# Kernel tuning notes

Hardware: AMD Instinct MI355X
Metric: run time of the kernel (lower is better)

The kernel has to match this reference:

```python
import jax, jax.numpy as jnp
import numpy as np

D_MODEL = 1024
N_HEADS = 16
HEAD_DIM = D_MODEL // N_HEADS
D_FF = 4096
EPS = 1e-5
THETA = 10000.0
B, S = 2, 2048


def _rope_cache(seq_len, head_dim, theta=THETA):
    inv_freq = 1.0 / theta ** (jnp.arange(0, head_dim, 2, dtype=jnp.float32) / head_dim)
    t = jnp.arange(seq_len, dtype=jnp.float32)
    freqs = jnp.einsum('i,j->ij', t, inv_freq)          # [S, head_dim//2]
    emb = jnp.concatenate([freqs, freqs], axis=-1)       # [S, head_dim]
    return jnp.cos(emb), jnp.sin(emb)


def _rotate_half(x):
    x1, x2 = jnp.split(x, 2, axis=-1)
    return jnp.concatenate([-x2, x1], axis=-1)


def _ada_rmsnorm(x, time_emb, weight, w1, b1, w2, b2):
    # time_mlp: Linear -> SiLU -> Linear producing [B, 2*D]
    h = jax.nn.silu(time_emb @ w1 + b1)
    scale, shift = jnp.split(h @ w2 + b2, 2, axis=-1)    # each [B, D]
    norm = x * jax.lax.rsqrt(jnp.mean(x * x, axis=-1, keepdims=True) + EPS)
    return norm * weight * (1.0 + scale[:, None, :]) + shift[:, None, :]


def setup_inputs() -> dict:
    key = jax.random.key(0)
    ks = jax.random.split(key, 24)
    rn = lambda k, shp: (jax.random.normal(k, shp, dtype=jnp.float32) * 0.02)
    return {
        'x': jax.random.normal(ks[0], (B, S, D_MODEL), dtype=jnp.float32),
        'time_emb': jax.random.normal(ks[1], (B, D_MODEL), dtype=jnp.float32),
        # norm1
        'w_norm1': jnp.ones((D_MODEL,), jnp.float32),
        't1_w1': rn(ks[2], (D_MODEL, D_MODEL)), 't1_b1': jnp.zeros((D_MODEL,), jnp.float32),
        't1_w2': rn(ks[3], (D_MODEL, 2 * D_MODEL)), 't1_b2': jnp.zeros((2 * D_MODEL,), jnp.float32),
        # norm2
        'w_norm2': jnp.ones((D_MODEL,), jnp.float32),
        't2_w1': rn(ks[4], (D_MODEL, D_MODEL)), 't2_b1': jnp.zeros((D_MODEL,), jnp.float32),
        't2_w2': rn(ks[5], (D_MODEL, 2 * D_MODEL)), 't2_b2': jnp.zeros((2 * D_MODEL,), jnp.float32),
        # attention projections (stored [in, out])
        'wq': rn(ks[6], (D_MODEL, D_MODEL)), 'bq': jnp.zeros((D_MODEL,), jnp.float32),
        'wk': rn(ks[7], (D_MODEL, D_MODEL)), 'bk': jnp.zeros((D_MODEL,), jnp.float32),
        'wv': rn(ks[8], (D_MODEL, D_MODEL)), 'bv': jnp.zeros((D_MODEL,), jnp.float32),
        'wo': rn(ks[9], (D_MODEL, D_MODEL)), 'bo': jnp.zeros((D_MODEL,), jnp.float32),
        # GLU FFN (no bias)
        'w_gate': rn(ks[10], (D_MODEL, D_FF)),
        'w_up': rn(ks[11], (D_MODEL, D_FF)),
        'w_down': rn(ks[12], (D_FF, D_MODEL)),
    }


def reference(x, time_emb,
              w_norm1, t1_w1, t1_b1, t1_w2, t1_b2,
              w_norm2, t2_w1, t2_b1, t2_w2, t2_b2,
              wq, bq, wk, bk, wv, bv, wo, bo,
              w_gate, w_up, w_down):
    b, s, _ = x.shape
    cos, sin = _rope_cache(s, HEAD_DIM)                  # [S, head_dim]

    # --- attention sub-block ---
    nx = _ada_rmsnorm(x, time_emb, w_norm1, t1_w1, t1_b1, t1_w2, t1_b2)
    q = (nx @ wq + bq).reshape(b, s, N_HEADS, HEAD_DIM)
    k = (nx @ wk + bk).reshape(b, s, N_HEADS, HEAD_DIM)
    v = (nx @ wv + bv).reshape(b, s, N_HEADS, HEAD_DIM)
    c = cos[:, None, :]  # [S,1,head_dim] broadcasts over heads
    si = sin[:, None, :]
    q = q * c + _rotate_half(q) * si
    k = k * c + _rotate_half(k) * si
    scores = jnp.einsum('bshd,bthd->bhst', q, k) / jnp.sqrt(jnp.float32(HEAD_DIM))
    probs = jax.nn.softmax(scores, axis=-1)
    attn = jnp.einsum('bhst,bthd->bshd', probs, v).reshape(b, s, D_MODEL)
    x = x + attn @ wo + bo

    # --- GLU FFN sub-block ---
    nx = _ada_rmsnorm(x, time_emb, w_norm2, t2_w1, t2_b1, t2_w2, t2_b2)
    gate = jax.nn.gelu(nx @ w_gate, approximate=False)
    ff = (gate * (nx @ w_up)) @ w_down
    return x + ff
```

## Files before the change

### kernel.cpp

```cpp
#include <hip/hip_runtime.h>
#include <hip/hip_bf16.h>

typedef __bf16 bf16_t;
typedef __bf16 bf16x8 __attribute__((ext_vector_type(8)));
typedef float f32x4 __attribute__((ext_vector_type(4)));

typedef __attribute__((address_space(3))) void lds_void_t;
typedef const __attribute__((address_space(1))) void gbl_void_t;

static constexpr int S_LEN = 2048;
static constexpr int NBATCH = 2;
static constexpr int DM = 1024;
static constexpr int NH = 16;
static constexpr int HD = 64;
static constexpr int DFF = 4096;
static constexpr int MROWS = NBATCH * S_LEN;
static constexpr int QKVN = 3072;

__global__ __launch_bounds__(256) void rope_table_k(float* __restrict__ cs) {
  int idx = blockIdx.x * 256 + threadIdx.x;
  int i = idx & 31, s = idx >> 5;
  float inv = powf(10000.0f, -(float)i / 32.0f);
  float ang = (float)s * inv;
  float c = cosf(ang), sn = sinf(ang);
  cs[s * 64 + i] = c;  cs[s * 64 + i + 32] = c;
  cs[S_LEN * 64 + s * 64 + i] = sn;  cs[S_LEN * 64 + s * 64 + i + 32] = sn;
}

__global__ __launch_bounds__(256) void gemv_k(const float* __restrict__ vin,
    const float* __restrict__ W, const float* __restrict__ bias,
    float* __restrict__ out, int N, int dosilu) {
  int b = blockIdx.y;
  int tj = threadIdx.x & 31, ti = threadIdx.x >> 5;
  int j = blockIdx.x * 32 + tj;
  const float* v = vin + b * DM;
  float acc = 0.f;
  int i0 = ti * 128;
#pragma unroll 8
  for (int i = i0; i < i0 + 128; ++i) acc += v[i] * W[(size_t)i * N + j];
  __shared__ float red[8][32];
  red[ti][tj] = acc;
  __syncthreads();
  if (threadIdx.x < 32) {
    float a = 0.f;
#pragma unroll
    for (int t = 0; t < 8; ++t) a += red[t][threadIdx.x];
    a += bias[j - tj + threadIdx.x];
    if (dosilu) a = a / (1.0f + expf(-a));
    out[(size_t)b * N + blockIdx.x * 32 + threadIdx.x] = a;
  }
}

template<typename T>
__global__ __launch_bounds__(256) void ada_rms_k(const T* __restrict__ x,
    const float* __restrict__ wnorm, const float* __restrict__ ss,
    bf16_t* __restrict__ out) {
  int row = blockIdx.x;
  int b = row >> 11;
  const T* xr = x + (size_t)row * DM;
  float xl[4]; float s = 0.f;
#pragma unroll
  for (int i = 0; i < 4; ++i) { xl[i] = (float)xr[threadIdx.x + i * 256]; s += xl[i] * xl[i]; }
#pragma unroll
  for (int d = 1; d < 64; d <<= 1) s += __shfl_xor(s, d);
  __shared__ float red[4];
  int w = threadIdx.x >> 6;
  if ((threadIdx.x & 63) == 0) red[w] = s;
  __syncthreads();
  s = red[0] + red[1] + red[2] + red[3];
  float r = rsqrtf(s * (1.0f / DM) + 1e-5f);
  bf16_t* orow = out + (size_t)row * DM;
#pragma unroll
  for (int i = 0; i < 4; ++i) {
    int j = threadIdx.x + i * 256;
    float sc = ss[b * 2048 + j], sh = ss[b * 2048 + 1024 + j];
    orow[j] = (bf16_t)(xl[i] * r * wnorm[j] * (1.0f + sc) + sh);
  }
}

__global__ __launch_bounds__(256) void prep_k(
    const float* __restrict__ wq, const float* __restrict__ wk,
    const float* __restrict__ wv, const float* __restrict__ wo,
    const float* __restrict__ wg, const float* __restrict__ wu,
    const float* __restrict__ wd,
    bf16_t* __restrict__ wqkvT, bf16_t* __restrict__ woT,
    bf16_t* __restrict__ wguT, bf16_t* __restrict__ wdT,
    const float* __restrict__ bq, const float* __restrict__ bk,
    const float* __restrict__ bv, float* __restrict__ bcat) {
  int id = blockIdx.x;
  if (id >= 16384) {
    int i = (id - 16384) * 256 + threadIdx.x;
    if (i < 3072)
      bcat[i] = i < 1024 ? bq[i] : (i < 2048 ? bk[i - 1024] : bv[i - 2048]);
    return;
  }
  const float* in; bf16_t* outp; int K, N, ilv, t;
  if (id < 4096) {
    int j = id >> 10; t = id & 1023; K = 1024; N = 1024; ilv = 0;
    in   = j == 0 ? wq : j == 1 ? wk : j == 2 ? wv : wo;
    outp = j == 3 ? woT : wqkvT + (size_t)j * 1024 * 1024;
  } else if (id < 12288) {
    int j = (id - 4096) >> 12; t = (id - 4096) & 4095; K = 1024; N = 4096;
    ilv = 1 + j; in = j ? wu : wg; outp = wguT;
  } else {
    t = id - 12288; K = 4096; N = 1024; ilv = 0; in = wd; outp = wdT;
  }
  int nbx = N >> 5;
  int n0 = (t % nbx) * 32, k0 = (t / nbx) * 32;
  __shared__ float tl[32][33];
  int tx = threadIdx.x & 31, ty = threadIdx.x >> 5;
#pragma unroll
  for (int i = 0; i < 32; i += 8)
    tl[ty + i][tx] = in[(size_t)(k0 + ty + i) * N + n0 + tx];
  __syncthreads();
#pragma unroll
  for (int i = 0; i < 32; i += 8) {
    int n = n0 + ty + i;
    int row = (ilv == 0) ? n : ((n >> 4) * 32 + (n & 15) + (ilv == 2 ? 16 : 0));
    outp[(size_t)row * K + k0 + tx] = (bf16_t)tl[tx][ty + i];
  }
}

template<int EPI, int BK>
__global__ __launch_bounds__((BK == 64) ? 512 : 256, (BK == 64) ? 4 : 1) void gemm_bt(
    const bf16_t* __restrict__ A, const bf16_t* __restrict__ BT,
    int M, int N, int K,
    const float* __restrict__ bias, const float* __restrict__ residf,
    const bf16_t* __restrict__ residb, bf16_t* outb, float* outf,
    const float* __restrict__ cstab, bf16_t* __restrict__ vt) {
  constexpr int DB = (BK == 64) ? 1 : 2;
  constexpr int BM = (BK == 64) ? 256 : 128;
  const int col0 = blockIdx.x * 128, row0 = blockIdx.y * BM;
  const int tid = threadIdx.x, l = tid & 63, w = tid >> 6;
  const int wr = (w >> 1) * 64, wc = (w & 1) * 64;
  const int lo = l & 15, hi = l >> 4;
  __shared__ __align__(16) bf16_t lA[DB][BM][BK];
  __shared__ __align__(16) bf16_t lB[DB][128][BK];
  f32x4 zero = {0.f, 0.f, 0.f, 0.f};
  f32x4 acc[4][4];
#pragma unroll
  for (int m = 0; m < 4; ++m)
#pragma unroll
    for (int n = 0; n < 4; ++n) acc[m][n] = zero;

  const int cmask = (BK == 64) ? (lo & 7) : lo;
  const int NT = K / BK;

  auto compute = [&](int buf) {
#pragma unroll
    for (int kk = 0; kk < BK; kk += 32) {
      bf16x8 af[4], bfr[4];
#pragma unroll
      for (int m = 0; m < 4; ++m)
        af[m] = *(const bf16x8*)&lA[buf][wr + m * 16 + lo][(((kk >> 3) + hi) ^ cmask) * 8];
#pragma unroll
      for (int n = 0; n < 4; ++n)
        bfr[n] = *(const bf16x8*)&lB[buf][wc + n * 16 + lo][(((kk >> 3) + hi) ^ cmask) * 8];
#pragma unroll
      for (int m = 0; m < 4; ++m)
#pragma unroll
        for (int n = 0; n < 4; ++n)
          acc[m][n] = __builtin_amdgcn_mfma_f32_16x16x32_bf16(af[m], bfr[n], acc[m][n], 0, 0, 0);
    }
  };

  if constexpr (DB == 1) {
    const int lrow = l >> 3;
    const int swzb = ((l & 7) ^ lrow) * 16;
    const char* pA[4]; const char* pB[2];
#pragma unroll
    for (int i = 0; i < 4; ++i)
      pA[i] = (const char*)&A[(size_t)(row0 + w * 32 + i * 8 + lrow) * K] + swzb;
#pragma unroll
    for (int i = 0; i < 2; ++i)
      pB[i] = (const char*)&BT[(size_t)(col0 + w * 16 + i * 8 + lrow) * K] + swzb;
    for (int t = 0; t < NT; ++t) {
      __syncthreads();
#pragma unroll
      for (int i = 0; i < 4; ++i) {
        __builtin_amdgcn_global_load_lds((gbl_void_t*)pA[i],
            (lds_void_t*)&lA[0][w * 32 + i * 8][0], 16, 0, 0);
        pA[i] += 128;
      }
#pragma unroll
      for (int i = 0; i < 2; ++i) {
        __builtin_amdgcn_global_load_lds((gbl_void_t*)pB[i],
            (lds_void_t*)&lB[0][w * 16 + i * 8][0], 16, 0, 0);
        pB[i] += 128;
      }
      __syncthreads();
      compute(0);
    }
  } else {
    const int lrow = l >> 4;
    const char* pA[8]; const char* pB[8];
#pragma unroll
    for (int i = 0; i < 8; ++i) {
      int rbase = w * 32 + i * 4;
      int key = (i * 4 + lrow) & 15;
      int swzb = ((l & 15) ^ key) * 16;
      pA[i] = (const char*)&A[(size_t)(row0 + rbase + lrow) * K] + swzb;
      pB[i] = (const char*)&BT[(size_t)(col0 + rbase + lrow) * K] + swzb;
    }
    auto stage_p = [&](int buf) {
#pragma unroll
      for (int i = 0; i < 8; ++i) {
        int rbase = w * 32 + i * 4;
        __builtin_amdgcn_global_load_lds((gbl_void_t*)pA[i], (lds_void_t*)&lA[buf][rbase][0], 16, 0, 0);
        __builtin_amdgcn_global_load_lds((gbl_void_t*)pB[i], (lds_void_t*)&lB[buf][rbase][0], 16, 0, 0);
        pA[i] += 256; pB[i] += 256;
      }
    };
    stage_p(0);
    __syncthreads();
    int cur = 0;
    for (int t = 0; t < NT; ++t) {
      if (t + 1 < NT) stage_p(cur ^ 1);
      compute(cur);
      __syncthreads();
      cur ^= 1;
    }
  }

  if (EPI == 5) {
    if (col0 >= 2048) {
#pragma unroll
      for (int m = 0; m < 4; ++m) {
#pragma unroll
        for (int n = 0; n < 4; ++n) {
          int cl = col0 + wc + n * 16 + lo;
          int r0 = row0 + wr + m * 16 + hi * 4;
          int dfull = cl - 2048;
          int bh = (r0 >> 11) * 16 + (dfull >> 6);
          int d = dfull & 63;
          float bb = bias[cl];
          __align__(8) bf16_t tmp[4];
#pragma unroll
          for (int j = 0; j < 4; ++j) tmp[j] = (bf16_t)(acc[m][n][j] + bb);
          *(uint2*)&vt[((size_t)bh * 64 + d) * S_LEN + (r0 & 2047)] = *(uint2*)tmp;
        }
      }
    } else {
#pragma unroll
      for (int m = 0; m < 4; ++m) {
#pragma unroll
        for (int n = 0; n < 2; ++n) {
          int cl = col0 + wc + n * 16 + lo;
          int i = cl & 63;
          float b1 = bias[cl], b2 = bias[cl + 32];
          float scale = (cl < 1024) ? 0.125f : 1.0f;
#pragma unroll
          for (int j = 0; j < 4; ++j) {
            int r = row0 + wr + m * 16 + hi * 4 + j;
            int s = r & 2047;
            float c = cstab[s * 64 + i], sn = cstab[S_LEN * 64 + s * 64 + i];
            float x1 = acc[m][n][j] + b1, x2 = acc[m][n + 2][j] + b2;
            size_t idx = (size_t)r * N + cl;
            outb[idx]      = (bf16_t)((x1 * c - x2 * sn) * scale);
            outb[idx + 32] = (bf16_t)((x2 * c + x1 * sn) * scale);
          }
        }
      }
    }
    return;
  }

  if (EPI == 6) {
#pragma unroll
    for (int m = 0; m < 4; ++m) {
#pragma unroll
      for (int p = 0; p < 2; ++p) {
        int clg = col0 + wc + 2 * p * 16;
        int jcol = ((clg >> 5) << 4) + lo;
#pragma unroll
        for (int j = 0; j < 4; ++j) {
          int r = row0 + wr + m * 16 + hi * 4 + j;
          float g = acc[m][2 * p][j];
          float u = acc[m][2 * p + 1][j];
          g = 0.5f * g * (1.0f + erff(g * 0.70710678118f));
          outb[(size_t)r * DFF + jcol] = (bf16_t)(g * u);
        }
      }
    }
    return;
  }

#pragma unroll
  for (int m = 0; m < 4; ++m) {
#pragma unroll
    for (int n = 0; n < 4; ++n) {
#pragma unroll
      for (int j = 0; j < 4; ++j) {
        int r = row0 + wr + m * 16 + hi * 4 + j;
        int cl = col0 + wc + n * 16 + lo;
        size_t idx = (size_t)r * N + cl;
        float vv = acc[m][n][j];
        if (EPI == 1)      { vv += bias[cl] + residf[idx]; outb[idx] = (bf16_t)vv; }
        else               { vv += (float)residb[idx]; outf[idx] = vv; }
      }
    }
  }
}

__global__ __launch_bounds__(512, 4) void attn_k(const bf16_t* __restrict__ qk,
    const bf16_t* __restrict__ vt, bf16_t* __restrict__ o) {
  int g = blockIdx.x;
  int orig = (g & 7) * 64 + (g >> 3);
  int qblk = orig & 15;
  int bh = orig >> 4;
  int b = bh >> 4, h = bh & 15;
  const int q0 = qblk * 128;
  const int tid = threadIdx.x, l = tid & 63, w = tid >> 6;
  const int lo = l & 15, hi = l >> 4;

  __shared__ __align__(16) bf16_t lk[128][72];
  __shared__ __align__(16) bf16_t lvt[64][136];
  __shared__ __align__(16) bf16_t lp[8][16][136];

  bf16x8 qf[2];
#pragma unroll
  for (int ks = 0; ks < 2; ++ks)
    qf[ks] = *(const bf16x8*)&qk[((size_t)(b * S_LEN) + q0 + w * 16 + lo) * QKVN
                                 + h * HD + ks * 32 + hi * 8];

  f32x4 zero = {0.f, 0.f, 0.f, 0.f};
  f32x4 oa[4];
#pragma unroll
  for (int n = 0; n < 4; ++n) oa[n] = zero;
  float mrow[4], lrow[4];
#pragma unroll
  for (int j = 0; j < 4; ++j) { mrow[j] = -1e30f; lrow[j] = 0.f; }

  const size_t kbase = (size_t)(b * S_LEN) * QKVN + 1024 + h * HD;
  const size_t vbase = (size_t)bh * 64 * S_LEN;

  for (int t0 = 0; t0 < S_LEN; t0 += 128) {
    __syncthreads();
#pragma unroll
    for (int it = 0; it < 2; ++it) {
      int idx = it * 512 + tid;
      int r = idx >> 3, dc = (idx & 7) * 8;
      *(uint4*)&lk[r][dc] = *(const uint4*)&qk[kbase + (size_t)(t0 + r) * QKVN + dc];
      int d = idx >> 4, sc = (idx & 15) * 8;
      *(uint4*)&lvt[d][sc] = *(const uint4*)&vt[vbase + (size_t)d * S_LEN + t0 + sc];
    }
    __syncthreads();

    f32x4 s[8];
#pragma unroll
    for (int n = 0; n < 8; ++n) s[n] = zero;
    __builtin_amdgcn_s_setprio(1);
#pragma unroll
    for (int ks = 0; ks < 2; ++ks) {
#pragma unroll
      for (int n = 0; n < 8; ++n) {
        bf16x8 bk = *(const bf16x8*)&lk[n * 16 + lo][ks * 32 + hi * 8];
        s[n] = __builtin_amdgcn_mfma_f32_16x16x32_bf16(qf[ks], bk, s[n], 0, 0, 0);
      }
    }
    __builtin_amdgcn_s_setprio(0);

#pragma unroll
    for (int j = 0; j < 4; ++j) {
      float mx = fmaxf(fmaxf(fmaxf(s[0][j], s[1][j]), fmaxf(s[2][j], s[3][j])),
                       fmaxf(fmaxf(s[4][j], s[5][j]), fmaxf(s[6][j], s[7][j])));
      mx = fmaxf(mx, __shfl_xor(mx, 1));
      mx = fmaxf(mx, __shfl_xor(mx, 2));
      mx = fmaxf(mx, __shfl_xor(mx, 4));
      mx = fmaxf(mx, __shfl_xor(mx, 8));
      if (__any(mx > mrow[j] + 8.0f)) {
        float mn = fmaxf(mrow[j], mx);
        float corr = __expf(mrow[j] - mn);
        mrow[j] = mn;
        lrow[j] *= corr;
#pragma unroll
        for (int n = 0; n < 4; ++n) oa[n][j] *= corr;
      }
      float psum = 0.f;
#pragma unroll
      for (int n = 0; n < 8; ++n) {
        float p = __expf(s[n][j] - mrow[j]);
        psum += p;
        lp[w][hi * 4 + j][n * 16 + lo] = (bf16_t)p;
      }
      lrow[j] += psum;
    }

    __builtin_amdgcn_s_setprio(1);
#pragma unroll
    for (int kk = 0; kk < 128; kk += 32) {
      bf16x8 ap = *(const bf16x8*)&lp[w][lo][kk + hi * 8];
#pragma unroll
      for (int n = 0; n < 4; ++n) {
        bf16x8 bv = *(const bf16x8*)&lvt[n * 16 + lo][kk + hi * 8];
        oa[n] = __builtin_amdgcn_mfma_f32_16x16x32_bf16(ap, bv, oa[n], 0, 0, 0);
      }
    }
    __builtin_amdgcn_s_setprio(0);
  }

#pragma unroll
  for (int j = 0; j < 4; ++j) {
    float ls = lrow[j];
    ls += __shfl_xor(ls, 1); ls += __shfl_xor(ls, 2);
    ls += __shfl_xor(ls, 4); ls += __shfl_xor(ls, 8);
    float inv = 1.0f / ls;
    int row = q0 + w * 16 + hi * 4 + j;
#pragma unroll
    for (int n = 0; n < 4; ++n)
      o[((size_t)(b * S_LEN) + row) * DM + h * HD + n * 16 + lo] = (bf16_t)(oa[n][j] * inv);
  }
}

extern "C" void kernel_launch(void* const* d_in, const int* in_sizes, int n_in,
                              void* d_out, int out_size, void* d_ws, size_t ws_size,
                              hipStream_t stream) {
  const float* x    = (const float*)d_in[0];
  const float* te   = (const float*)d_in[1];
  const float* wn1  = (const float*)d_in[2];
  const float* t1w1 = (const float*)d_in[3];
  const float* t1b1 = (const float*)d_in[4];
  const float* t1w2 = (const float*)d_in[5];
  const float* t1b2 = (const float*)d_in[6];
  const float* wn2  = (const float*)d_in[7];
  const float* t2w1 = (const float*)d_in[8];
  const float* t2b1 = (const float*)d_in[9];
  const float* t2w2 = (const float*)d_in[10];
  const float* t2b2 = (const float*)d_in[11];
  const float* wq   = (const float*)d_in[12];
  const float* bq   = (const float*)d_in[13];
  const float* wk   = (const float*)d_in[14];
  const float* bk   = (const float*)d_in[15];
  const float* wv   = (const float*)d_in[16];
  const float* bv   = (const float*)d_in[17];
  const float* wo   = (const float*)d_in[18];
  const float* bo   = (const float*)d_in[19];
  const float* wg   = (const float*)d_in[20];
  const float* wu   = (const float*)d_in[21];
  const float* wd   = (const float*)d_in[22];
  float* out = (float*)d_out;

  char* ws = (char*)d_ws;
  const size_t MB = 1ull << 20;
  bf16_t* woT   = (bf16_t*)(ws + 0 * MB);
  bf16_t* wguT  = (bf16_t*)(ws + 2 * MB);
  bf16_t* wdT   = (bf16_t*)(ws + 18 * MB);
  bf16_t* nx    = (bf16_t*)(ws + 26 * MB);
  bf16_t* wqkvT = (bf16_t*)(ws + 34 * MB);
  bf16_t* qkvb  = (bf16_t*)(ws + 40 * MB);
  bf16_t* vt    = (bf16_t*)(ws + 64 * MB);
  bf16_t* gb    = (bf16_t*)(ws + 40 * MB);
  bf16_t* attnb = (bf16_t*)(ws + 72 * MB);
  bf16_t* x2b   = (bf16_t*)(ws + 80 * MB);
  float*  cs    = (float*)(ws + 88 * MB);
  float*  ss1   = (float*)(ws + 89 * MB);
  float*  ss2   = (float*)(ws + 89 * MB + 16384);
  float*  htmp  = (float*)(ws + 89 * MB + 32768);
  float*  bcat  = (float*)(ws + 89 * MB + 40960);

  rope_table_k<<<256, 256, 0, stream>>>(cs);
  gemv_k<<<dim3(32, 2), 256, 0, stream>>>(te, t1w1, t1b1, htmp, 1024, 1);
  gemv_k<<<dim3(64, 2), 256, 0, stream>>>(htmp, t1w2, t1b2, ss1, 2048, 0);
  gemv_k<<<dim3(32, 2), 256, 0, stream>>>(te, t2w1, t2b1, htmp, 1024, 1);
  gemv_k<<<dim3(64, 2), 256, 0, stream>>>(htmp, t2w2, t2b2, ss2, 2048, 0);

  prep_k<<<16396, 256, 0, stream>>>(wq, wk, wv, wo, wg, wu, wd,
                                    wqkvT, woT, wguT, wdT, bq, bk, bv, bcat);

  ada_rms_k<float><<<MROWS, 256, 0, stream>>>(x, wn1, ss1, nx);

  gemm_bt<5, 64><<<dim3(24, 16), 512, 0, stream>>>(nx, wqkvT, MROWS, QKVN, DM,
                                                   bcat, nullptr, nullptr, qkvb, nullptr, cs, vt);

  attn_k<<<512, 512, 0, stream>>>(qkvb, vt, attnb);

  gemm_bt<1, 128><<<dim3(8, 32), 256, 0, stream>>>(attnb, woT, MROWS, DM, DM,
                                                   bo, x, nullptr, x2b, nullptr, nullptr, nullptr);

  ada_rms_k<bf16_t><<<MROWS, 256, 0, stream>>>(x2b, wn2, ss2, nx);

  gemm_bt<6, 64><<<dim3(64, 16), 512, 0, stream>>>(nx, wguT, MROWS, 2 * DFF, DM,
                                                   nullptr, nullptr, nullptr, gb, nullptr, nullptr, nullptr);
  gemm_bt<4, 128><<<dim3(8, 32), 256, 0, stream>>>(gb, wdT, MROWS, DM, DFF,
                                                   nullptr, nullptr, x2b, nullptr, out, nullptr, nullptr);
}
```

Before: 321.7 us.

## Split attention KV tile across warp pairs with 32-row query tiles and merge

Each attention warp now handles 32 query rows and half of each 128-key tile, instead of 16 rows over the full tile. K and V fragments loaded from LDS are reused across two query sub-tiles, which halves the LDS fragment reads per MFMA. At the end, the two warp groups merge their partial softmax states (max, sum, output) through a shared buffer that aliases the K/V storage. The cost is more registers per thread, an extra synchronised reduction step, and a larger LDS allocation.

```diff
diff --git a/kernel.cpp b/kernel.cpp
--- a/kernel.cpp
+++ b/kernel.cpp
@@ -312,24 +312,35 @@
   const int q0 = qblk * 128;
   const int tid = threadIdx.x, l = tid & 63, w = tid >> 6;
   const int lo = l & 15, hi = l >> 4;
-
-  __shared__ __align__(16) bf16_t lk[128][72];
-  __shared__ __align__(16) bf16_t lvt[64][136];
-  __shared__ __align__(16) bf16_t lp[8][16][136];
-
-  bf16x8 qf[2];
-#pragma unroll
-  for (int ks = 0; ks < 2; ++ks)
-    qf[ks] = *(const bf16x8*)&qk[((size_t)(b * S_LEN) + q0 + w * 16 + lo) * QKVN
-                                 + h * HD + ks * 32 + hi * 8];
+  const int wq = w & 3, koff = (w >> 2) * 64;
+  const int rb = q0 + wq * 32;
+
+  __shared__ __align__(16) char smem[72704];
+  bf16_t (*lk)[72]   = (bf16_t(*)[72])smem;
+  bf16_t (*lvt)[136] = (bf16_t(*)[136])(smem + 18432);
+  bf16_t (*lp)[72]   = (bf16_t(*)[72])(smem + 35840);
+  float* obuf = (float*)smem;
+  float* mlb  = (float*)(smem + 32768);
+
+  bf16x8 qf[2][2];
+#pragma unroll
+  for (int m = 0; m < 2; ++m)
+#pragma unroll
+    for (int ks = 0; ks < 2; ++ks)
+      qf[m][ks] = *(const bf16x8*)&qk[((size_t)(b * S_LEN) + rb + m * 16 + lo) * QKVN
+                                      + h * HD + ks * 32 + hi * 8];
 
   f32x4 zero = {0.f, 0.f, 0.f, 0.f};
-  f32x4 oa[4];
-#pragma unroll
-  for (int n = 0; n < 4; ++n) oa[n] = zero;
-  float mrow[4], lrow[4];
-#pragma unroll
-  for (int j = 0; j < 4; ++j) { mrow[j] = -1e30f; lrow[j] = 0.f; }
+  f32x4 oa[2][4];
+#pragma unroll
+  for (int m = 0; m < 2; ++m)
+#pragma unroll
+    for (int n = 0; n < 4; ++n) oa[m][n] = zero;
+  float mrow[2][4], lrow[2][4];
+#pragma unroll
+  for (int m = 0; m < 2; ++m)
+#pragma unroll
+    for (int j = 0; j < 4; ++j) { mrow[m][j] = -1e30f; lrow[m][j] = 0.f; }
 
   const size_t kbase = (size_t)(b * S_LEN) * QKVN + 1024 + h * HD;
   const size_t vbase = (size_t)bh * 64 * S_LEN;
@@ -346,69 +357,115 @@
     }
     __syncthreads();
 
-    f32x4 s[8];
-#pragma unroll
-    for (int n = 0; n < 8; ++n) s[n] = zero;
+    f32x4 s[2][4];
+#pragma unroll
+    for (int m = 0; m < 2; ++m)
+#pragma unroll
+      for (int n = 0; n < 4; ++n) s[m][n] = zero;
     __builtin_amdgcn_s_setprio(1);
 #pragma unroll
     for (int ks = 0; ks < 2; ++ks) {
-#pragma unroll
-      for (int n = 0; n < 8; ++n) {
-        bf16x8 bk = *(const bf16x8*)&lk[n * 16 + lo][ks * 32 + hi * 8];
-        s[n] = __builtin_amdgcn_mfma_f32_16x16x32_bf16(qf[ks], bk, s[n], 0, 0, 0);
-      }
+      bf16x8 bk[4];
+#pragma unroll
+      for (int n = 0; n < 4; ++n) bk[n] = *(const bf16x8*)&lk[koff + n * 16 + lo][ks * 32 + hi * 8];
+#pragma unroll
+      for (int m = 0; m < 2; ++m)
+#pragma unroll
+        for (int n = 0; n < 4; ++n)
+          s[m][n] = __builtin_amdgcn_mfma_f32_16x16x32_bf16(qf[m][ks], bk[n], s[m][n], 0, 0, 0);
     }
     __builtin_amdgcn_s_setprio(0);
 
 #pragma unroll
+    for (int m = 0; m < 2; ++m) {
+#pragma unroll
+      for (int j = 0; j < 4; ++j) {
+        float mx = fmaxf(fmaxf(s[m][0][j], s[m][1][j]), fmaxf(s[m][2][j], s[m][3][j]));
+        mx = fmaxf(mx, __shfl_xor(mx, 1));
+        mx = fmaxf(mx, __shfl_xor(mx, 2));
+        mx = fmaxf(mx, __shfl_xor(mx, 4));
+        mx = fmaxf(mx, __shfl_xor(mx, 8));
+        if (__any(mx > mrow[m][j] + 8.0f)) {
+          float mn = fmaxf(mrow[m][j], mx);
+          float corr = __expf(mrow[m][j] - mn);
+          mrow[m][j] = mn;
+          lrow[m][j] *= corr;
+#pragma unroll
+          for (int n = 0; n < 4; ++n) oa[m][n][j] *= corr;
+        }
+        float psum = 0.f;
+#pragma unroll
+        for (int n = 0; n < 4; ++n) {
+          float p = __expf(s[m][n][j] - mrow[m][j]);
+          psum += p;
+          lp[w * 32 + m * 16 + hi * 4 + j][n * 16 + lo] = (bf16_t)p;
+        }
+        lrow[m][j] += psum;
+      }
+    }
+
+    __builtin_amdgcn_s_setprio(1);
+#pragma unroll
+    for (int kk = 0; kk < 64; kk += 32) {
+      bf16x8 ap[2], bv[4];
+#pragma unroll
+      for (int m = 0; m < 2; ++m) ap[m] = *(const bf16x8*)&lp[w * 32 + m * 16 + lo][kk + hi * 8];
+#pragma unroll
+      for (int n = 0; n < 4; ++n) bv[n] = *(const bf16x8*)&lvt[n * 16 + lo][koff + kk + hi * 8];
+#pragma unroll
+      for (int m = 0; m < 2; ++m)
+#pragma unroll
+        for (int n = 0; n < 4; ++n)
+          oa[m][n] = __builtin_amdgcn_mfma_f32_16x16x32_bf16(ap[m], bv[n], oa[m][n], 0, 0, 0);
+    }
+    __builtin_amdgcn_s_setprio(0);
+  }
+
+  float lsum[2][4];
+#pragma unroll
+  for (int m = 0; m < 2; ++m)
+#pragma unroll
     for (int j = 0; j < 4; ++j) {
-      float mx = fmaxf(fmaxf(fmaxf(s[0][j], s[1][j]), fmaxf(s[2][j], s[3][j])),
-                       fmaxf(fmaxf(s[4][j], s[5][j]), fmaxf(s[6][j], s[7][j])));
-      mx = fmaxf(mx, __shfl_xor(mx, 1));
-      mx = fmaxf(mx, __shfl_xor(mx, 2));
-      mx = fmaxf(mx, __shfl_xor(mx, 4));
-      mx = fmaxf(mx, __shfl_xor(mx, 8));
-      if (__any(mx > mrow[j] + 8.0f)) {
-        float mn = fmaxf(mrow[j], mx);
-        float corr = __expf(mrow[j] - mn);
-        mrow[j] = mn;
-        lrow[j] *= corr;
-#pragma unroll
-        for (int n = 0; n < 4; ++n) oa[n][j] *= corr;
-      }
-      float psum = 0.f;
-#pragma unroll
-      for (int n = 0; n < 8; ++n) {
-        float p = __expf(s[n][j] - mrow[j]);
-        psum += p;
-        lp[w][hi * 4 + j][n * 16 + lo] = (bf16_t)p;
-      }
-      lrow[j] += psum;
-    }
-
-    __builtin_amdgcn_s_setprio(1);
-#pragma unroll
-    for (int kk = 0; kk < 128; kk += 32) {
-      bf16x8 ap = *(const bf16x8*)&lp[w][lo][kk + hi * 8];
-#pragma unroll
-      for (int n = 0; n < 4; ++n) {
-        bf16x8 bv = *(const bf16x8*)&lvt[n * 16 + lo][kk + hi * 8];
-        oa[n] = __builtin_amdgcn_mfma_f32_16x16x32_bf16(ap, bv, oa[n], 0, 0, 0);
-      }
-    }
-    __builtin_amdgcn_s_setprio(0);
-  }
-
-#pragma unroll
-  for (int j = 0; j < 4; ++j) {
-    float ls = lrow[j];
-    ls += __shfl_xor(ls, 1); ls += __shfl_xor(ls, 2);
-    ls += __shfl_xor(ls, 4); ls += __shfl_xor(ls, 8);
-    float inv = 1.0f / ls;
-    int row = q0 + w * 16 + hi * 4 + j;
-#pragma unroll
-    for (int n = 0; n < 4; ++n)
-      o[((size_t)(b * S_LEN) + row) * DM + h * HD + n * 16 + lo] = (bf16_t)(oa[n][j] * inv);
+      float ls = lrow[m][j];
+      ls += __shfl_xor(ls, 1); ls += __shfl_xor(ls, 2);
+      ls += __shfl_xor(ls, 4); ls += __shfl_xor(ls, 8);
+      lsum[m][j] = ls;
+    }
+
+  __syncthreads();
+  if (w < 4) {
+    float* ob = obuf + (size_t)wq * 32 * 64;
+#pragma unroll
+    for (int m = 0; m < 2; ++m)
+#pragma unroll
+      for (int j = 0; j < 4; ++j) {
+        int r = m * 16 + hi * 4 + j;
+#pragma unroll
+        for (int n = 0; n < 4; ++n) ob[r * 64 + n * 16 + lo] = oa[m][n][j];
+        mlb[wq * 64 + r] = mrow[m][j];
+        mlb[wq * 64 + 32 + r] = lsum[m][j];
+      }
+  }
+  __syncthreads();
+  if (w >= 4) {
+    const float* ob = obuf + (size_t)wq * 32 * 64;
+#pragma unroll
+    for (int m = 0; m < 2; ++m)
+#pragma unroll
+      for (int j = 0; j < 4; ++j) {
+        int r = m * 16 + hi * 4 + j;
+        float m1 = mlb[wq * 64 + r], l1 = mlb[wq * 64 + 32 + r];
+        float m2 = mrow[m][j], l2 = lsum[m][j];
+        float mm = fmaxf(m1, m2);
+        float e1 = __expf(m1 - mm), e2 = __expf(m2 - mm);
+        float inv = 1.0f / (l1 * e1 + l2 * e2);
+        int row = rb + r;
+#pragma unroll
+        for (int n = 0; n < 4; ++n) {
+          float num = ob[r * 64 + n * 16 + lo] * e1 + oa[m][n][j] * e2;
+          o[((size_t)(b * S_LEN) + row) * DM + h * HD + n * 16 + lo] = (bf16_t)(num * inv);
+        }
+      }
   }
 }
 
```

Result: slower. 354.1 us (+10.1%).
